# Kernel optimization log

Measured on AMD Instinct MI355X. Metric: run time of the kernel, lower is better.

Reference implementation:

```python
import jax, jax.numpy as jnp
import numpy as np

B, C, H, W = 16, 192, 64, 64
L = 256           # number of quantization levels (len(sos.unique_values))
EXTREMA = 10.0    # codebook support roughly [-extrema, extrema]


def setup_inputs() -> dict:
    key = jax.random.key(0)
    k1, k2, k3 = jax.random.split(key, 3)
    inputs = jax.random.normal(k1, (B, C, H, W), dtype=jnp.float32) * 3.0
    means = jax.random.normal(k2, (B, C, H, W), dtype=jnp.float32)
    # sorted codebook of unique quantizer output values (sos.unique_values)
    raw = jax.random.uniform(k3, (L,), dtype=jnp.float32,
                             minval=-EXTREMA, maxval=EXTREMA)
    unique_values = jnp.sort(raw)
    return {"inputs": inputs, "means": means, "unique_values": unique_values}


def _nearest_symbols(v, unique_values):
    # Parallel binary search over the sorted codebook; equivalent to the
    # original per-element argmin(|keys - x|) in transform_map.
    L_ = unique_values.shape[0]
    idx = jnp.searchsorted(unique_values, v)          # in [0, L]
    idx = jnp.clip(idx, 1, L_ - 1)
    left = unique_values[idx - 1]
    right = unique_values[idx]
    # on ties, argmin picks the lower index -> use <=
    return jnp.where(jnp.abs(v - left) <= jnp.abs(v - right), idx - 1, idx)


def reference(inputs, means, unique_values):
    # quantize(mode='symbols'): subtract means, snap to nearest codebook
    # value, map value -> integer symbol via the sorted codebook.
    v = inputs - means
    symbols = _nearest_symbols(v, unique_values)      # int32 [B,C,H,W]
    # dequantize: symbol -> float codebook value (map_cdf_sos), add means.
    dequant = unique_values[symbols] + means          # float32 [B,C,H,W]
    return dequant, symbols
```

## Files before the change

kernel.cpp:

```cpp
#include <hip/hip_runtime.h>


#define LVL 256
#define NB  1024
#define QPT 4

__device__ __forceinline__ int bucket_of(float v, float lo, float scale) {
    int b = (int)floorf((v - lo) * scale);
    return min(max(b, 0), NB - 1);
}

__global__ __launch_bounds__(256) void agc_build_lut(
    const float* __restrict__ uv, float4* __restrict__ lutA, float4* __restrict__ lutB)
{
    __shared__ float s_uv[LVL];
    __shared__ int   s_b[LVL];
    int t = threadIdx.x;
    s_uv[t] = uv[t];
    __syncthreads();
    const float lo    = s_uv[0];
    const float scale = (float)NB / (s_uv[LVL - 1] - lo);
    s_b[t] = bucket_of(s_uv[t], lo, scale);
    __syncthreads();

    int b = blockIdx.x * 256 + t;
    if (b >= NB) return;

    int A = 0, cnt = 0;
    for (int j = 0; j < LVL; ++j) {
        int bj = s_b[j];
        A   += (bj <  b);
        cnt += (bj == b);
    }

    const float INF = __builtin_inff();
    float4 ea, eb;
    if (cnt == 0) {
        int idx = min(max(A, 1), LVL - 1);
        ea = make_float4(INF, INF, s_uv[idx - 1], s_uv[idx]);
        eb = make_float4(0.f, 0.f, 0.f, __int_as_float(idx - 1));
    } else if (cnt <= 2 && A >= 1 && A + cnt <= LVL - 1) {
        float p0 = s_uv[A];
        float p1 = (cnt >= 2) ? s_uv[A + 1] : INF;
        float c0 = s_uv[A - 1];
        float c1 = s_uv[A];
        float c2 = s_uv[A + 1];
        float c3 = (A + 2 <= LVL - 1) ? s_uv[A + 2] : 0.f;
        ea = make_float4(p0, p1, c0, c1);
        eb = make_float4(c2, c3, 0.f, __int_as_float(A - 1));
    } else {
        ea = make_float4(0.f, 0.f, 0.f, 0.f);
        eb = make_float4(0.f, 0.f, 0.f, __int_as_float(-(A + 1)));
    }
    lutA[b] = ea;
    lutB[b] = eb;
}

__global__ __launch_bounds__(256) void agc_quant_lut(
    const float* __restrict__ inputs,
    const float* __restrict__ means,
    const float* __restrict__ uv,
    const float4* __restrict__ lutA,
    const float4* __restrict__ lutB,
    float* __restrict__ out_deq,
    float* __restrict__ out_sym,
    int n4, int n, int nfull)
{
    __shared__ float  s_uv[LVL];
    __shared__ float4 s_A[NB];
    __shared__ float4 s_B[NB];

    int t = threadIdx.x;
    s_uv[t] = uv[t];
    #pragma unroll
    for (int q = 0; q < NB / 256; ++q) {
        int j = q * 256 + t;
        s_A[j] = lutA[j];
        s_B[j] = lutB[j];
    }
    __syncthreads();

    const float lo    = s_uv[0];
    const float scale = (float)NB / (s_uv[LVL - 1] - lo);

    const int i0 = blockIdx.x * (256 * QPT) + t;
    const bool full = (blockIdx.x < nfull);

    float4 in[QPT], mn[QPT];
    if (full) {
        #pragma unroll
        for (int k = 0; k < QPT; ++k) {
            int i = i0 + k * 256;
            in[k] = reinterpret_cast<const float4*>(inputs)[i];
            mn[k] = reinterpret_cast<const float4*>(means)[i];
        }
    } else {
        #pragma unroll
        for (int k = 0; k < QPT; ++k) {
            int i = i0 + k * 256;
            if (i < n4) {
                in[k] = reinterpret_cast<const float4*>(inputs)[i];
                mn[k] = reinterpret_cast<const float4*>(means)[i];
            }
        }
    }

    #pragma unroll
    for (int k = 0; k < QPT; ++k) {
        int i = i0 + k * 256;
        if (!full && i >= n4) continue;

        float vs[4] = {in[k].x - mn[k].x, in[k].y - mn[k].y,
                       in[k].z - mn[k].z, in[k].w - mn[k].w};
        float ms[4] = {mn[k].x, mn[k].y, mn[k].z, mn[k].w};
        float dq[4], sy[4];

        #pragma unroll
        for (int e = 0; e < 4; ++e) {
            float v = vs[e];
            int b = bucket_of(v, lo, scale);

            float4 A4 = s_A[b];
            float4 B4 = s_B[b];
            int bp = __float_as_int(B4.w);

            float left, right;
            int base;
            if (bp >= 0) {
                int sel = (A4.x < v) + (A4.y < v);
                left  = (sel == 0) ? A4.z : ((sel == 1) ? A4.w : B4.x);
                right = (sel == 0) ? A4.w : ((sel == 1) ? B4.x : B4.y);
                base  = bp + sel;
            } else {
                int s = -bp - 1;
                while (s < LVL && s_uv[s] < v) ++s;
                int idx = min(max(s, 1), LVL - 1);
                left  = s_uv[idx - 1];
                right = s_uv[idx];
                base  = idx - 1;
            }

            bool tl = (fabsf(v - left) <= fabsf(v - right));
            sy[e] = (float)(base + (tl ? 0 : 1));
            dq[e] = (tl ? left : right) + ms[e];
        }

        reinterpret_cast<float4*>(out_deq)[i] = make_float4(dq[0], dq[1], dq[2], dq[3]);
        reinterpret_cast<float4*>(out_sym)[i] = make_float4(sy[0], sy[1], sy[2], sy[3]);
    }

    if (blockIdx.x == 0 && t == 0) {
        for (int j = n4 * 4; j < n; ++j) {
            float m = means[j];
            float v = inputs[j] - m;
            int l = 0, h = LVL;
            for (int s = 0; s < 8; ++s) {
                int mm = (l + h) >> 1;
                bool r = (s_uv[mm] < v);
                l = r ? (mm + 1) : l;
                h = r ? h : mm;
            }
            int idx = min(max(l, 1), LVL - 1);
            float left = s_uv[idx - 1], right = s_uv[idx];
            bool tl = fabsf(v - left) <= fabsf(v - right);
            out_deq[j] = (tl ? left : right) + m;
            out_sym[j] = (float)(tl ? idx - 1 : idx);
        }
    }
}

__global__ __launch_bounds__(256) void agc_quant_fallback(
    const float* __restrict__ inputs,
    const float* __restrict__ means,
    const float* __restrict__ uv,
    float* __restrict__ out_deq,
    float* __restrict__ out_sym,
    int n4, int n)
{
    __shared__ float s_uv[LVL];
    s_uv[threadIdx.x] = uv[threadIdx.x];
    __syncthreads();

    int i = blockIdx.x * blockDim.x + threadIdx.x;
    if (i < n4) {
        float4 in = reinterpret_cast<const float4*>(inputs)[i];
        float4 mn = reinterpret_cast<const float4*>(means)[i];
        float vs[4] = {in.x - mn.x, in.y - mn.y, in.z - mn.z, in.w - mn.w};
        float ms[4] = {mn.x, mn.y, mn.z, mn.w};
        float dq[4], sy[4];
        #pragma unroll
        for (int k = 0; k < 4; ++k) {
            float v = vs[k];
            int lo = 0, hi = LVL;
            #pragma unroll
            for (int s = 0; s < 8; ++s) {
                int mid = (lo + hi) >> 1;
                bool r = (s_uv[mid] < v);
                lo = r ? (mid + 1) : lo;
                hi = r ? hi : mid;
            }
            int idx = min(max(lo, 1), LVL - 1);
            float left = s_uv[idx - 1], right = s_uv[idx];
            bool tl = (fabsf(v - left) <= fabsf(v - right));
            sy[k] = (float)(tl ? idx - 1 : idx);
            dq[k] = (tl ? left : right) + ms[k];
        }
        reinterpret_cast<float4*>(out_deq)[i] = make_float4(dq[0], dq[1], dq[2], dq[3]);
        reinterpret_cast<float4*>(out_sym)[i] = make_float4(sy[0], sy[1], sy[2], sy[3]);
    }
    if (blockIdx.x == 0 && threadIdx.x == 0) {
        for (int j = n4 * 4; j < n; ++j) {
            float m = means[j];
            float v = inputs[j] - m;
            int lo = 0, hi = LVL;
            for (int s = 0; s < 8; ++s) {
                int mid = (lo + hi) >> 1;
                bool r = (s_uv[mid] < v);
                lo = r ? (mid + 1) : lo;
                hi = r ? hi : mid;
            }
            int idx = min(max(lo, 1), LVL - 1);
            float left = s_uv[idx - 1], right = s_uv[idx];
            bool tl = fabsf(v - left) <= fabsf(v - right);
            out_deq[j] = (tl ? left : right) + m;
            out_sym[j] = (float)(tl ? idx - 1 : idx);
        }
    }
}

extern "C" void kernel_launch(void* const* d_in, const int* in_sizes, int n_in,
                              void* d_out, int out_size, void* d_ws, size_t ws_size,
                              hipStream_t stream)
{
    const float* inputs = (const float*)d_in[0];
    const float* means  = (const float*)d_in[1];
    const float* uv     = (const float*)d_in[2];

    int n  = in_sizes[0];
    int n4 = n / 4;

    float* out     = (float*)d_out;
    float* out_deq = out;
    float* out_sym = out + n;

    size_t need = (size_t)NB * 2 * sizeof(float4);
    if (d_ws != nullptr && ws_size >= need) {
        float4* lutA = (float4*)d_ws;
        float4* lutB = lutA + NB;
        agc_build_lut<<<NB / 256, 256, 0, stream>>>(uv, lutA, lutB);

        int per_blk = 256 * QPT;
        int nfull   = n4 / per_blk;
        int blocks  = (n4 + per_blk - 1) / per_blk;
        if (blocks < 1) blocks = 1;
        agc_quant_lut<<<blocks, 256, 0, stream>>>(
            inputs, means, uv, lutA, lutB,
            out_deq, out_sym, n4, n, nfull);
    } else {
        int blocks = (n4 + 255) / 256;
        if (blocks < 1) blocks = 1;
        agc_quant_fallback<<<blocks, 256, 0, stream>>>(
            inputs, means, uv, out_deq, out_sym, n4, n);
    }
}
```

Baseline: 188.3 us.

## Read LUT directly from global memory instead of staging into shared memory

Removes the per-block copy of the bucket lookup tables and codebook into shared memory, gathering LUT entries straight from global memory (relying on caches) and batching the four gathers per vector before use. Halves the bucket count to shrink the table, and switches input loads to nontemporal loads. This eliminates a large per-block prologue and barrier and frees LDS for occupancy, at the cost of uncached-latency gathers and slightly more buckets needing the linear-scan fallback.

```diff
diff --git a/kernel.cpp b/kernel.cpp
--- a/kernel.cpp
+++ b/kernel.cpp
@@ -2,8 +2,10 @@
 
 
 #define LVL 256
-#define NB  1024
+#define NB  512
 #define QPT 4
+
+typedef float f32x4 __attribute__((ext_vector_type(4)));
 
 __device__ __forceinline__ int bucket_of(float v, float lo, float scale) {
     int b = (int)floorf((v - lo) * scale);
@@ -60,47 +62,34 @@
     const float* __restrict__ inputs,
     const float* __restrict__ means,
     const float* __restrict__ uv,
-    const float4* __restrict__ lutA,
-    const float4* __restrict__ lutB,
+    const f32x4* __restrict__ lutA,
+    const f32x4* __restrict__ lutB,
     float* __restrict__ out_deq,
     float* __restrict__ out_sym,
     int n4, int n, int nfull)
 {
-    __shared__ float  s_uv[LVL];
-    __shared__ float4 s_A[NB];
-    __shared__ float4 s_B[NB];
+    const float lo    = uv[0];
+    const float scale = (float)NB / (uv[LVL - 1] - lo);
 
     int t = threadIdx.x;
-    s_uv[t] = uv[t];
-    #pragma unroll
-    for (int q = 0; q < NB / 256; ++q) {
-        int j = q * 256 + t;
-        s_A[j] = lutA[j];
-        s_B[j] = lutB[j];
-    }
-    __syncthreads();
-
-    const float lo    = s_uv[0];
-    const float scale = (float)NB / (s_uv[LVL - 1] - lo);
-
     const int i0 = blockIdx.x * (256 * QPT) + t;
     const bool full = (blockIdx.x < nfull);
 
-    float4 in[QPT], mn[QPT];
+    f32x4 in[QPT], mn[QPT];
     if (full) {
         #pragma unroll
         for (int k = 0; k < QPT; ++k) {
             int i = i0 + k * 256;
-            in[k] = reinterpret_cast<const float4*>(inputs)[i];
-            mn[k] = reinterpret_cast<const float4*>(means)[i];
+            in[k] = __builtin_nontemporal_load(reinterpret_cast<const f32x4*>(inputs) + i);
+            mn[k] = __builtin_nontemporal_load(reinterpret_cast<const f32x4*>(means) + i);
         }
     } else {
         #pragma unroll
         for (int k = 0; k < QPT; ++k) {
             int i = i0 + k * 256;
             if (i < n4) {
-                in[k] = reinterpret_cast<const float4*>(inputs)[i];
-                mn[k] = reinterpret_cast<const float4*>(means)[i];
+                in[k] = __builtin_nontemporal_load(reinterpret_cast<const f32x4*>(inputs) + i);
+                mn[k] = __builtin_nontemporal_load(reinterpret_cast<const f32x4*>(means) + i);
             }
         }
     }
@@ -115,28 +104,35 @@
         float ms[4] = {mn[k].x, mn[k].y, mn[k].z, mn[k].w};
         float dq[4], sy[4];
 
+        int bx[4];
+        #pragma unroll
+        for (int e = 0; e < 4; ++e) bx[e] = bucket_of(vs[e], lo, scale);
+
+        f32x4 A4[4], B4[4];
+        #pragma unroll
+        for (int e = 0; e < 4; ++e) {
+            A4[e] = lutA[bx[e]];
+            B4[e] = lutB[bx[e]];
+        }
+
         #pragma unroll
         for (int e = 0; e < 4; ++e) {
             float v = vs[e];
-            int b = bucket_of(v, lo, scale);
-
-            float4 A4 = s_A[b];
-            float4 B4 = s_B[b];
-            int bp = __float_as_int(B4.w);
+            int bp = __float_as_int(B4[e].w);
 
             float left, right;
             int base;
             if (bp >= 0) {
-                int sel = (A4.x < v) + (A4.y < v);
-                left  = (sel == 0) ? A4.z : ((sel == 1) ? A4.w : B4.x);
-                right = (sel == 0) ? A4.w : ((sel == 1) ? B4.x : B4.y);
+                int sel = (A4[e].x < v) + (A4[e].y < v);
+                left  = (sel == 0) ? A4[e].z : ((sel == 1) ? A4[e].w : B4[e].x);
+                right = (sel == 0) ? A4[e].w : ((sel == 1) ? B4[e].x : B4[e].y);
                 base  = bp + sel;
             } else {
                 int s = -bp - 1;
-                while (s < LVL && s_uv[s] < v) ++s;
+                while (s < LVL && uv[s] < v) ++s;
                 int idx = min(max(s, 1), LVL - 1);
-                left  = s_uv[idx - 1];
-                right = s_uv[idx];
+                left  = uv[idx - 1];
+                right = uv[idx];
                 base  = idx - 1;
             }
 
@@ -156,12 +152,12 @@
             int l = 0, h = LVL;
             for (int s = 0; s < 8; ++s) {
                 int mm = (l + h) >> 1;
-                bool r = (s_uv[mm] < v);
+                bool r = (uv[mm] < v);
                 l = r ? (mm + 1) : l;
                 h = r ? h : mm;
             }
             int idx = min(max(l, 1), LVL - 1);
-            float left = s_uv[idx - 1], right = s_uv[idx];
+            float left = uv[idx - 1], right = uv[idx];
             bool tl = fabsf(v - left) <= fabsf(v - right);
             out_deq[j] = (tl ? left : right) + m;
             out_sym[j] = (float)(tl ? idx - 1 : idx);
@@ -247,14 +243,14 @@
     if (d_ws != nullptr && ws_size >= need) {
         float4* lutA = (float4*)d_ws;
         float4* lutB = lutA + NB;
-        agc_build_lut<<<NB / 256, 256, 0, stream>>>(uv, lutA, lutB);
+        agc_build_lut<<<(NB + 255) / 256, 256, 0, stream>>>(uv, lutA, lutB);
 
         int per_blk = 256 * QPT;
         int nfull   = n4 / per_blk;
         int blocks  = (n4 + per_blk - 1) / per_blk;
         if (blocks < 1) blocks = 1;
         agc_quant_lut<<<blocks, 256, 0, stream>>>(
-            inputs, means, uv, lutA, lutB,
+            inputs, means, uv, (const f32x4*)lutA, (const f32x4*)lutB,
             out_deq, out_sym, n4, n, nfull);
     } else {
         int blocks = (n4 + 255) / 256;
```

New measurement: 199.4 us. 5.9% more time.
